# Kernel tuning notes

Hardware: AMD Instinct MI355X
Metric: run time of the kernel (lower is better)

## Reference

```python
import jax, jax.numpy as jnp
import numpy as np


def _rope_tables(T, half):
    # theta_i = 10000^(-i/half), standard RoPE frequencies for head_size=2*half
    thetas = 10000.0 ** (-jnp.arange(half, dtype=jnp.float32) / half)  # (half,)
    ang = jnp.arange(T, dtype=jnp.float32)[:, None] * thetas[None, :]  # (T, half)
    return jnp.sin(ang), jnp.cos(ang)


def _apply_rope(x, sin, cos):
    # x: (B, H, T, hs); sin/cos: (T, hs//2). Interleaved pair rotation.
    xe = x[..., 0::2]
    xo = x[..., 1::2]
    s = sin[None, None, :, :]
    c = cos[None, None, :, :]
    re = xe * c - xo * s
    ro = xe * s + xo * c
    return jnp.stack([re, ro], axis=-1).reshape(x.shape)


def setup_inputs() -> dict:
    key = jax.random.key(0)
    ks = jax.random.split(key, 5)
    B, T, C, H = 4, 2048, 1024, 16
    scale = 1.0 / np.sqrt(C)
    x = jax.random.normal(ks[0], (B, T, C), dtype=jnp.float32)
    Wqkv = jax.random.normal(ks[1], (C, 3 * C), dtype=jnp.float32) * scale
    bqkv = jax.random.normal(ks[2], (3 * C,), dtype=jnp.float32) * 0.01
    Wout = jax.random.normal(ks[3], (C, C), dtype=jnp.float32) * scale
    bout = jax.random.normal(ks[4], (C,), dtype=jnp.float32) * 0.01
    return {"x": x, "Wqkv": Wqkv, "bqkv": bqkv, "Wout": Wout, "bout": bout,
            "num_heads": H}


def reference(x, Wqkv, bqkv, Wout, bout, num_heads) -> jnp.ndarray:
    B, T, C = x.shape
    H = num_heads
    hs = C // H
    norm = 1.0 / np.sqrt(hs)

    qkv = x @ Wqkv + bqkv                       # (B, T, 3C)
    qkv = qkv.reshape(B, T, 3, H, hs)
    qkv = jnp.transpose(qkv, (0, 3, 2, 1, 4))   # (B, H, 3, T, hs) = transpose(1,3)
    q, k, v = qkv[:, :, 0], qkv[:, :, 1], qkv[:, :, 2]  # each (B, H, T, hs)

    sin, cos = _rope_tables(T, hs // 2)
    q = _apply_rope(q, sin, cos)
    k = _apply_rope(k, sin, cos)

    att = jnp.einsum('bhqd,bhkd->bhqk', q, k) * norm  # (B, H, T, T)
    causal = jnp.triu(jnp.ones((T, T), dtype=bool), k=1)
    att = jnp.where(causal[None, None], -jnp.inf, att)
    att_prob = jax.nn.softmax(att, axis=-1)

    out = jnp.einsum('bhqk,bhkd->bhqd', att_prob, v)  # (B, H, T, hs)
    out = jnp.transpose(out, (0, 2, 1, 3)).reshape(B, T, C)
    return out @ Wout + bout
```

## Files before the change

kernel.cpp:

```cpp
#include <hip/hip_runtime.h>
#include <math.h>

#define B_   4
#define T_   2048
#define C_   1024
#define H_   16
#define HS   64
#define HALF 32
#define QKV_N (3 * C_)
#define M_    (B_ * T_)

using bf16x8 = __attribute__((ext_vector_type(8))) short;
using f32x4  = __attribute__((ext_vector_type(4))) float;
using f32x16 = __attribute__((ext_vector_type(16))) float;
using u16x4  = __attribute__((ext_vector_type(4))) unsigned short;

__device__ __forceinline__ unsigned short f2bf(float f) {
    unsigned u = __builtin_bit_cast(unsigned, f);
    u = (u + 0x7FFFu + ((u >> 16) & 1u)) >> 16;
    return (unsigned short)u;
}
__device__ __forceinline__ float bf2f(unsigned short b) {
    return __builtin_bit_cast(float, (unsigned)b << 16);
}
__device__ __forceinline__ unsigned cvtpk_bf16(float lo, float hi_) {
    unsigned r;
    asm("v_cvt_pk_bf16_f32 %0, %1, %2" : "=v"(r) : "v"(lo), "v"(hi_));
    return r;
}
__device__ __forceinline__ void gload16(const void* g, void* l) {
    __builtin_amdgcn_global_load_lds(
        (const __attribute__((address_space(1))) unsigned int*)g,
        (__attribute__((address_space(3))) unsigned int*)l, 16, 0, 0);
}
#define WAIT_VMCNT_8() asm volatile("s_waitcnt vmcnt(8)" ::: "memory")
#define WAIT_VMCNT_0() asm volatile("s_waitcnt vmcnt(0)" ::: "memory")

__global__ __launch_bounds__(256) void prep_kernel(
    const float* __restrict__ in, unsigned short* __restrict__ out,
    float2* __restrict__ tab)
{
    const int bid = blockIdx.x;
    if (bid < 4096) {
        const size_t i = ((size_t)bid * 256 + threadIdx.x) * 8;
        const float4 a = *reinterpret_cast<const float4*>(&in[i]);
        const float4 b = *reinterpret_cast<const float4*>(&in[i + 4]);
        bf16x8 v;
        v[0] = f2bf(a.x); v[1] = f2bf(a.y); v[2] = f2bf(a.z); v[3] = f2bf(a.w);
        v[4] = f2bf(b.x); v[5] = f2bf(b.y); v[6] = f2bf(b.z); v[7] = f2bf(b.w);
        *reinterpret_cast<bf16x8*>(&out[i]) = v;
    } else {
        const int idx = (bid - 4096) * 256 + threadIdx.x;
        const int t = idx / HALF;
        const int i = idx % HALF;
        const float theta = powf(10000.0f, -(float)i / (float)HALF);
        const float ang = (float)t * theta;
        float sn, cs;
        sincosf(ang, &sn, &cs);
        tab[idx] = make_float2(sn, cs);
    }
}

__global__ __launch_bounds__(256) void wtrans_kernel(
    const float* __restrict__ Wqkv, const float* __restrict__ Wout,
    unsigned short* __restrict__ Wqkvt, unsigned short* __restrict__ Woutt)
{
    __shared__ float tile[32][33];
    const int bid = blockIdx.x;
    const float* W;
    unsigned short* Wt;
    int N, k0, n0;
    if (bid < 3072) {
        W = Wqkv; Wt = Wqkvt; N = QKV_N;
        n0 = (bid % 96) * 32; k0 = (bid / 96) * 32;
    } else {
        const int r2 = bid - 3072;
        W = Wout; Wt = Woutt; N = C_;
        n0 = (r2 % 32) * 32; k0 = (r2 / 32) * 32;
    }
    const int K = C_;
    const int r = threadIdx.x / 32;
    const int c = threadIdx.x % 32;
    #pragma unroll
    for (int it = 0; it < 4; ++it)
        tile[r + it * 8][c] = W[(size_t)(k0 + r + it * 8) * N + n0 + c];
    __syncthreads();
    #pragma unroll
    for (int it = 0; it < 4; ++it)
        Wt[(size_t)(n0 + r + it * 8) * K + k0 + c] = f2bf(tile[c][r + it * 8]);
}

template <int N, int K, bool BF16OUT, bool ROPE, bool VSPLIT>
__global__ __launch_bounds__(256, 4) void gemm_mfma_kernel(
    const unsigned short* __restrict__ A, const unsigned short* __restrict__ Bt,
    const float* __restrict__ bias, const float2* __restrict__ tab,
    void* __restrict__ Cout, unsigned short* __restrict__ vt, int nbx, int nby)
{
    __shared__ unsigned short As[128 * 32];
    __shared__ unsigned short Bs[128 * 32];

    const int tid  = threadIdx.x;
    const int lane = tid & 63;
    const int wave = tid >> 6;
    const int wr   = wave >> 1;
    const int wc   = wave & 1;
    const int l15  = lane & 15;
    const int l4   = lane >> 4;

    const int bid  = blockIdx.x;
    const int xcd  = bid & 7;
    const int w    = bid >> 3;
    const int cpr  = nbx >> 1;
    const int rpr  = nby >> 2;
    const int by   = ((xcd >> 1) * rpr) + (w / cpr);
    const int bx   = ((xcd & 1) * cpr) + (w % cpr);
    const int row0 = by * 128;
    const int col0 = bx * 128;

    f32x4 acc[4][4] = {};

    const int ar = tid >> 2, ac = (tid & 3) * 8;
    const unsigned short* ap = &A[(size_t)(row0 + ar) * K + ac];
    const unsigned short* bp = &Bt[(size_t)(col0 + ar) * K + ac];

    for (int it = 0; it < K / 32; ++it) {
        gload16(ap,          &As[tid * 8]);
        gload16(ap + 64 * K, &As[(tid + 256) * 8]);
        gload16(bp,          &Bs[tid * 8]);
        gload16(bp + 64 * K, &Bs[(tid + 256) * 8]);
        __syncthreads();

        bf16x8 a[4], b[4];
        #pragma unroll
        for (int mi = 0; mi < 4; ++mi)
            a[mi] = *reinterpret_cast<const bf16x8*>(
                &As[(wr * 64 + mi * 16 + l15) * 32 + l4 * 8]);
        #pragma unroll
        for (int nj = 0; nj < 4; ++nj)
            b[nj] = *reinterpret_cast<const bf16x8*>(
                &Bs[(wc * 64 + nj * 16 + l15) * 32 + l4 * 8]);
        #pragma unroll
        for (int mi = 0; mi < 4; ++mi)
            #pragma unroll
            for (int nj = 0; nj < 4; ++nj)
                acc[mi][nj] = __builtin_amdgcn_mfma_f32_16x16x32_bf16(
                    a[mi], b[nj], acc[mi][nj], 0, 0, 0);
        __syncthreads();
        ap += 32;
        bp += 32;
    }

    float bv[4];
    #pragma unroll
    for (int nj = 0; nj < 4; ++nj)
        bv[nj] = bias[col0 + wc * 64 + nj * 16 + l15];

    if (VSPLIT && col0 >= 2 * C_) {
        #pragma unroll
        for (int mi = 0; mi < 4; ++mi) {
            const int rowb = row0 + wr * 64 + mi * 16 + l4 * 4;
            const int b  = rowb >> 11;
            const int t0 = rowb & (T_ - 1);
            #pragma unroll
            for (int nj = 0; nj < 4; ++nj) {
                const int cv = col0 - 2 * C_ + wc * 64 + nj * 16 + l15;
                u16x4 pack;
                #pragma unroll
                for (int r = 0; r < 4; ++r)
                    pack[r] = f2bf(acc[mi][nj][r] + bv[nj]);
                *reinterpret_cast<u16x4*>(
                    &vt[((size_t)(b * H_ * HS + cv)) * T_ + t0]) = pack;
            }
        }
        return;
    }

    const bool doRope = ROPE && (col0 < 2 * C_);

    #pragma unroll
    for (int mi = 0; mi < 4; ++mi) {
        #pragma unroll
        for (int r = 0; r < 4; ++r) {
            const int row = row0 + wr * 64 + mi * 16 + l4 * 4 + r;
            const int t   = row & (T_ - 1);
            #pragma unroll
            for (int nj = 0; nj < 4; ++nj) {
                const int col = col0 + wc * 64 + nj * 16 + l15;
                float v = acc[mi][nj][r] + bv[nj];
                if (doRope) {
                    const float partner = __shfl_xor(v, 1);
                    const float2 sc = tab[t * HALF + ((col & 63) >> 1)];
                    v = v * sc.y + ((col & 1) ? partner : -partner) * sc.x;
                }
                if (BF16OUT)
                    ((unsigned short*)Cout)[(size_t)row * N + col] = f2bf(v);
                else
                    ((float*)Cout)[(size_t)row * N + col] = v;
            }
        }
    }
}

__global__ __launch_bounds__(256, 2) void attn_mfma4_kernel(
    const unsigned short* __restrict__ qkv,
    const unsigned short* __restrict__ vt,
    unsigned short* __restrict__ out)
{
    __shared__ unsigned short Ks[2][128 * 64];
    __shared__ unsigned short Vs[2][64 * 128];

    const int idx = blockIdx.x;
    const int bh  = idx & 63;
    const int qp  = idx >> 6;
    const int b   = bh >> 4;
    const int h   = bh & 15;
    const int qtA = qp;
    const int qtB = 15 - qp;

    const int tid  = threadIdx.x;
    const int lane = tid & 63;
    const int w    = tid >> 6;
    const int l31  = lane & 31;
    const int hi   = lane >> 5;

    const int qwA = qtA * 128 + w * 32;
    const int qgA = qwA + l31;
    const int qwB = qtB * 128 + w * 32;
    const int qgB = qwB + l31;

    bf16x8 aqA[4], aqB[4];
    {
        const unsigned short* qpA = &qkv[(size_t)(b * T_ + qgA) * QKV_N + h * HS + hi * 8];
        const unsigned short* qpB = &qkv[(size_t)(b * T_ + qgB) * QKV_N + h * HS + hi * 8];
        #pragma unroll
        for (int kc = 0; kc < 4; ++kc) {
            aqA[kc] = *reinterpret_cast<const bf16x8*>(qpA + kc * 16);
            aqB[kc] = *reinterpret_cast<const bf16x8*>(qpB + kc * 16);
        }
    }

    f32x16 accA0 = {}, accA1 = {}, accB0 = {}, accB1 = {};
    float mA = -INFINITY, lA = 0.f, mB = -INFINITY, lB = 0.f;

    const float SCALE = 0.18033688011112042f;

    auto stageKV = [&](int buf, int it) {
        #pragma unroll
        for (int n = 0; n < 4; ++n) {
            const int r  = n * 32 + (tid >> 3);
            const int sk = ((tid & 7) ^ (r & 7)) * 8;
            gload16(&qkv[(size_t)(b * T_ + it * 128 + r) * QKV_N + C_ + h * HS + sk],
                    &Ks[buf][(n * 256 + tid) * 8]);
        }
        #pragma unroll
        for (int n = 0; n < 4; ++n) {
            const int d  = n * 16 + (tid >> 4);
            const int sv = ((tid & 15) ^ (d & 7)) * 8;
            gload16(&vt[((size_t)(bh * HS + d)) * T_ + it * 128 + sv],
                    &Vs[buf][(n * 256 + tid) * 8]);
        }
    };

    auto process = [&](const unsigned short* Kb, const unsigned short* Vb,
                       const bf16x8* aq, f32x16& a0, f32x16& a1,
                       float& mval, float& lval, int qw, int qg,
                       int sub, int kbase) {
        f32x16 st0 = {}, st1 = {};
        #pragma unroll
        for (int kc = 0; kc < 4; ++kc) {
            const int bo = kc * 32 + hi * 16;
            const int r0 = sub * 64 + l31;
            const bf16x8 ak0 = *reinterpret_cast<const bf16x8*>(
                &Kb[r0 * 64 + ((bo ^ ((r0 & 7) << 4)) >> 1)]);
            st0 = __builtin_amdgcn_mfma_f32_32x32x16_bf16(ak0, aq[kc], st0, 0, 0, 0);
            const int r1 = r0 + 32;
            const bf16x8 ak1 = *reinterpret_cast<const bf16x8*>(
                &Kb[r1 * 64 + ((bo ^ ((r1 & 7) << 4)) >> 1)]);
            st1 = __builtin_amdgcn_mfma_f32_32x32x16_bf16(ak1, aq[kc], st1, 0, 0, 0);
        }

        float p[32];
        if (kbase + 63 > qw) {
            #pragma unroll
            for (int r = 0; r < 16; ++r) {
                const int j0 = kbase + (r & 3) + 8 * (r >> 2) + 4 * hi;
                p[r]      = (j0      <= qg) ? st0[r] * SCALE : -INFINITY;
                p[r + 16] = (j0 + 32 <= qg) ? st1[r] * SCALE : -INFINITY;
            }
        } else {
            #pragma unroll
            for (int r = 0; r < 16; ++r) {
                p[r]      = st0[r] * SCALE;
                p[r + 16] = st1[r] * SCALE;
            }
        }

        float tm = p[0];
        #pragma unroll
        for (int r = 1; r < 32; ++r) tm = fmaxf(tm, p[r]);
        tm = fmaxf(tm, __shfl_xor(tm, 32));

        const bool upd = (tm > mval + 8.f);
        if (__ballot(upd)) {
            const float nm = upd ? tm : mval;
            const float sf = exp2f(mval - nm);
            lval *= sf;
            #pragma unroll
            for (int r = 0; r < 16; ++r) { a0[r] *= sf; a1[r] *= sf; }
            mval = nm;
        }

        float rs = 0.f;
        #pragma unroll
        for (int r = 0; r < 32; ++r) { p[r] = exp2f(p[r] - mval); rs += p[r]; }
        rs += __shfl_xor(rs, 32);
        lval += rs;

        #pragma unroll
        for (int jt = 0; jt < 2; ++jt) {
            #pragma unroll
            for (int c = 0; c < 2; ++c) {
                const int base = jt * 16 + c * 8;
                const unsigned pa = cvtpk_bf16(p[base + 0], p[base + 1]);
                const unsigned pb = cvtpk_bf16(p[base + 2], p[base + 3]);
                const unsigned pc = cvtpk_bf16(p[base + 4], p[base + 5]);
                const unsigned pd = cvtpk_bf16(p[base + 6], p[base + 7]);
                const unsigned pas = (unsigned)__shfl_xor((int)pa, 32);
                const unsigned pbs = (unsigned)__shfl_xor((int)pb, 32);
                const unsigned pcs = (unsigned)__shfl_xor((int)pc, 32);
                const unsigned pds = (unsigned)__shfl_xor((int)pd, 32);
                int4 bw;
                bw.x = (int)(hi ? pcs : pa);
                bw.y = (int)(hi ? pds : pb);
                bw.z = (int)(hi ? pc  : pas);
                bw.w = (int)(hi ? pd  : pbs);
                const bf16x8 bfrag = __builtin_bit_cast(bf16x8, bw);

                const int lslot = sub * 8 + (jt * 2 + c) * 2 + hi;
                const int d0 = l31;
                const bf16x8 av0 = *reinterpret_cast<const bf16x8*>(
                    &Vb[d0 * 128 + (lslot ^ (d0 & 7)) * 8]);
                a0 = __builtin_amdgcn_mfma_f32_32x32x16_bf16(av0, bfrag, a0, 0, 0, 0);
                const int d1 = 32 + l31;
                const bf16x8 av1 = *reinterpret_cast<const bf16x8*>(
                    &Vb[d1 * 128 + (lslot ^ (d1 & 7)) * 8]);
                a1 = __builtin_amdgcn_mfma_f32_32x32x16_bf16(av1, bfrag, a1, 0, 0, 0);
            }
        }
    };

    const int nIter = qtB + 1;
    stageKV(0, 0);
    for (int it = 0; it < nIter; ++it) {
        const int cur = it & 1;
        __builtin_amdgcn_sched_barrier(0);
        if (it + 1 < nIter) {
            stageKV(cur ^ 1, it + 1);
            WAIT_VMCNT_8();
        } else {
            WAIT_VMCNT_0();
        }
        __builtin_amdgcn_s_barrier();
        __builtin_amdgcn_sched_barrier(0);

        const unsigned short* Kb = &Ks[cur][0];
        const unsigned short* Vb = &Vs[cur][0];
        #pragma unroll
        for (int sub = 0; sub < 2; ++sub) {
            const int kbase = it * 128 + sub * 64;
            if (kbase <= qwA + 31)
                process(Kb, Vb, aqA, accA0, accA1, mA, lA, qwA, qgA, sub, kbase);
            if (kbase <= qwB + 31)
                process(Kb, Vb, aqB, accB0, accB1, mB, lB, qwB, qgB, sub, kbase);
        }
        __builtin_amdgcn_sched_barrier(0);
        __builtin_amdgcn_s_barrier();
    }

    {
        const float inv = 1.0f / lA;
        unsigned short* orow = &out[(size_t)(b * T_ + qgA) * C_ + h * HS];
        #pragma unroll
        for (int g = 0; g < 4; ++g) {
            uint2 wv;
            wv.x = cvtpk_bf16(accA0[4 * g + 0] * inv, accA0[4 * g + 1] * inv);
            wv.y = cvtpk_bf16(accA0[4 * g + 2] * inv, accA0[4 * g + 3] * inv);
            *reinterpret_cast<uint2*>(&orow[8 * g + 4 * hi]) = wv;
            uint2 wv1;
            wv1.x = cvtpk_bf16(accA1[4 * g + 0] * inv, accA1[4 * g + 1] * inv);
            wv1.y = cvtpk_bf16(accA1[4 * g + 2] * inv, accA1[4 * g + 3] * inv);
            *reinterpret_cast<uint2*>(&orow[32 + 8 * g + 4 * hi]) = wv1;
        }
    }
    {
        const float inv = 1.0f / lB;
        unsigned short* orow = &out[(size_t)(b * T_ + qgB) * C_ + h * HS];
        #pragma unroll
        for (int g = 0; g < 4; ++g) {
            uint2 wv;
            wv.x = cvtpk_bf16(accB0[4 * g + 0] * inv, accB0[4 * g + 1] * inv);
            wv.y = cvtpk_bf16(accB0[4 * g + 2] * inv, accB0[4 * g + 3] * inv);
            *reinterpret_cast<uint2*>(&orow[8 * g + 4 * hi]) = wv;
            uint2 wv1;
            wv1.x = cvtpk_bf16(accB1[4 * g + 0] * inv, accB1[4 * g + 1] * inv);
            wv1.y = cvtpk_bf16(accB1[4 * g + 2] * inv, accB1[4 * g + 3] * inv);
            *reinterpret_cast<uint2*>(&orow[32 + 8 * g + 4 * hi]) = wv1;
        }
    }
}

extern "C" void kernel_launch(void* const* d_in, const int* in_sizes, int n_in,
                              void* d_out, int out_size, void* d_ws, size_t ws_size,
                              hipStream_t stream)
{
    const float* x    = (const float*)d_in[0];
    const float* Wqkv = (const float*)d_in[1];
    const float* bqkv = (const float*)d_in[2];
    const float* Wout = (const float*)d_in[3];
    const float* bout = (const float*)d_in[4];
    float* out = (float*)d_out;

    char* ws = (char*)d_ws;
    unsigned short* qkvb  = (unsigned short*)ws;
    unsigned short* xb    = (unsigned short*)(ws + 50331648);
    unsigned short* attnb = (unsigned short*)(ws + 67108864);
    unsigned short* vt_g  = (unsigned short*)(ws + 83886080);
    unsigned short* Wqkvt = (unsigned short*)(ws + 100663296);
    unsigned short* Woutt = (unsigned short*)(ws + 106954752);
    float2* tab           = (float2*)(ws + 109051904);

    prep_kernel<<<4352, 256, 0, stream>>>(x, xb, tab);
    wtrans_kernel<<<4096, 256, 0, stream>>>(Wqkv, Wout, Wqkvt, Woutt);

    gemm_mfma_kernel<QKV_N, C_, true, true, true>
        <<<(M_ / 128) * (QKV_N / 128), 256, 0, stream>>>(
        xb, Wqkvt, bqkv, tab, qkvb, vt_g, QKV_N / 128, M_ / 128);

    attn_mfma4_kernel<<<B_ * H_ * (T_ / 256), 256, 0, stream>>>(qkvb, vt_g, attnb);

    gemm_mfma_kernel<C_, C_, false, false, false>
        <<<(M_ / 128) * (C_ / 128), 256, 0, stream>>>(
        attnb, Woutt, bout, nullptr, out, nullptr, C_ / 128, M_ / 128);
}
```

Measured before the change: 189.6 us.

## Process full 128-key tiles per softmax step and fold Q scale into QKV GEMM

The attention inner step now computes a full 128-key score tile (four MFMA accumulators) per online-softmax update instead of two 64-key halves, halving the number of max/rescale passes. The softmax scale is folded into Q during the QKV GEMM epilogue, which removes per-element multiplies in attention. It also uses hardware exp2, max3 reductions, permlane32_swap in place of cross-half shuffles, and s_setprio around MFMA bursts. The larger score tile raises register pressure under the 2-blocks-per-CU launch bound.

```diff
diff --git a/kernel.cpp b/kernel.cpp
--- a/kernel.cpp
+++ b/kernel.cpp
@@ -14,6 +14,7 @@
 using f32x4  = __attribute__((ext_vector_type(4))) float;
 using f32x16 = __attribute__((ext_vector_type(16))) float;
 using u16x4  = __attribute__((ext_vector_type(4))) unsigned short;
+using u32x2  = __attribute__((ext_vector_type(2))) unsigned int;
 
 __device__ __forceinline__ unsigned short f2bf(float f) {
     unsigned u = __builtin_bit_cast(unsigned, f);
@@ -35,6 +36,15 @@
 }
 #define WAIT_VMCNT_8() asm volatile("s_waitcnt vmcnt(8)" ::: "memory")
 #define WAIT_VMCNT_0() asm volatile("s_waitcnt vmcnt(0)" ::: "memory")
+
+#if __has_builtin(__builtin_amdgcn_exp2f)
+#define EXP2(x) __builtin_amdgcn_exp2f(x)
+#else
+#define EXP2(x) exp2f(x)
+#endif
+#define FMAX3(a, b, c) fmaxf(fmaxf((a), (b)), (c))
+
+#define QSCALE 0.18033688011112042f
 
 __global__ __launch_bounds__(256) void prep_kernel(
     const float* __restrict__ in, unsigned short* __restrict__ out,
@@ -176,6 +186,7 @@
     }
 
     const bool doRope = ROPE && (col0 < 2 * C_);
+    const bool doScaleQ = ROPE && (col0 < C_);
 
     #pragma unroll
     for (int mi = 0; mi < 4; ++mi) {
@@ -192,6 +203,7 @@
                     const float2 sc = tab[t * HALF + ((col & 63) >> 1)];
                     v = v * sc.y + ((col & 1) ? partner : -partner) * sc.x;
                 }
+                if (doScaleQ) v *= QSCALE;
                 if (BF16OUT)
                     ((unsigned short*)Cout)[(size_t)row * N + col] = f2bf(v);
                 else
@@ -201,7 +213,7 @@
     }
 }
 
-__global__ __launch_bounds__(256, 2) void attn_mfma4_kernel(
+__global__ __launch_bounds__(256, 2) void attn_mfma5_kernel(
     const unsigned short* __restrict__ qkv,
     const unsigned short* __restrict__ vt,
     unsigned short* __restrict__ out)
@@ -242,8 +254,6 @@
     f32x16 accA0 = {}, accA1 = {}, accB0 = {}, accB1 = {};
     float mA = -INFINITY, lA = 0.f, mB = -INFINITY, lB = 0.f;
 
-    const float SCALE = 0.18033688011112042f;
-
     auto stageKV = [&](int buf, int it) {
         #pragma unroll
         for (int n = 0; n < 4; ++n) {
@@ -263,88 +273,110 @@
 
     auto process = [&](const unsigned short* Kb, const unsigned short* Vb,
                        const bf16x8* aq, f32x16& a0, f32x16& a1,
-                       float& mval, float& lval, int qw, int qg,
-                       int sub, int kbase) {
-        f32x16 st0 = {}, st1 = {};
+                       float& mval, float& lval, int qw, int qg, int kbase) {
+        f32x16 s[4] = {};
+        __builtin_amdgcn_s_setprio(1);
         #pragma unroll
         for (int kc = 0; kc < 4; ++kc) {
             const int bo = kc * 32 + hi * 16;
-            const int r0 = sub * 64 + l31;
-            const bf16x8 ak0 = *reinterpret_cast<const bf16x8*>(
-                &Kb[r0 * 64 + ((bo ^ ((r0 & 7) << 4)) >> 1)]);
-            st0 = __builtin_amdgcn_mfma_f32_32x32x16_bf16(ak0, aq[kc], st0, 0, 0, 0);
-            const int r1 = r0 + 32;
-            const bf16x8 ak1 = *reinterpret_cast<const bf16x8*>(
-                &Kb[r1 * 64 + ((bo ^ ((r1 & 7) << 4)) >> 1)]);
-            st1 = __builtin_amdgcn_mfma_f32_32x32x16_bf16(ak1, aq[kc], st1, 0, 0, 0);
-        }
-
-        float p[32];
-        if (kbase + 63 > qw) {
-            #pragma unroll
-            for (int r = 0; r < 16; ++r) {
-                const int j0 = kbase + (r & 3) + 8 * (r >> 2) + 4 * hi;
-                p[r]      = (j0      <= qg) ? st0[r] * SCALE : -INFINITY;
-                p[r + 16] = (j0 + 32 <= qg) ? st1[r] * SCALE : -INFINITY;
+            #pragma unroll
+            for (int g = 0; g < 4; ++g) {
+                const int rj = g * 32 + l31;
+                const bf16x8 ak = *reinterpret_cast<const bf16x8*>(
+                    &Kb[rj * 64 + ((bo ^ ((rj & 7) << 4)) >> 1)]);
+                s[g] = __builtin_amdgcn_mfma_f32_32x32x16_bf16(ak, aq[kc], s[g], 0, 0, 0);
             }
-        } else {
-            #pragma unroll
-            for (int r = 0; r < 16; ++r) {
-                p[r]      = st0[r] * SCALE;
-                p[r + 16] = st1[r] * SCALE;
+        }
+        __builtin_amdgcn_s_setprio(0);
+
+        if (kbase + 127 > qw) {
+            #pragma unroll
+            for (int g = 0; g < 4; ++g) {
+                #pragma unroll
+                for (int r = 0; r < 16; ++r) {
+                    const int j0 = kbase + g * 32 + (r & 3) + 8 * (r >> 2) + 4 * hi;
+                    if (j0 > qg) s[g][r] = -INFINITY;
+                }
             }
         }
 
-        float tm = p[0];
-        #pragma unroll
-        for (int r = 1; r < 32; ++r) tm = fmaxf(tm, p[r]);
+        float tg[4];
+        #pragma unroll
+        for (int g = 0; g < 4; ++g) {
+            const float v0 = FMAX3(s[g][0],  s[g][1],  s[g][2]);
+            const float v1 = FMAX3(s[g][3],  s[g][4],  s[g][5]);
+            const float v2 = FMAX3(s[g][6],  s[g][7],  s[g][8]);
+            const float v3 = FMAX3(s[g][9],  s[g][10], s[g][11]);
+            const float v4 = FMAX3(s[g][12], s[g][13], s[g][14]);
+            tg[g] = fmaxf(FMAX3(v0, v1, v2), FMAX3(v3, v4, s[g][15]));
+        }
+        float tm = fmaxf(fmaxf(tg[0], tg[1]), fmaxf(tg[2], tg[3]));
         tm = fmaxf(tm, __shfl_xor(tm, 32));
 
         const bool upd = (tm > mval + 8.f);
         if (__ballot(upd)) {
             const float nm = upd ? tm : mval;
-            const float sf = exp2f(mval - nm);
+            const float sf = EXP2(mval - nm);
             lval *= sf;
             #pragma unroll
             for (int r = 0; r < 16; ++r) { a0[r] *= sf; a1[r] *= sf; }
             mval = nm;
         }
 
-        float rs = 0.f;
-        #pragma unroll
-        for (int r = 0; r < 32; ++r) { p[r] = exp2f(p[r] - mval); rs += p[r]; }
+        float rs0 = 0.f, rs1 = 0.f, rs2 = 0.f, rs3 = 0.f;
+        #pragma unroll
+        for (int r = 0; r < 16; ++r) {
+            s[0][r] = EXP2(s[0][r] - mval); rs0 += s[0][r];
+            s[1][r] = EXP2(s[1][r] - mval); rs1 += s[1][r];
+            s[2][r] = EXP2(s[2][r] - mval); rs2 += s[2][r];
+            s[3][r] = EXP2(s[3][r] - mval); rs3 += s[3][r];
+        }
+        float rs = (rs0 + rs1) + (rs2 + rs3);
         rs += __shfl_xor(rs, 32);
         lval += rs;
 
         #pragma unroll
-        for (int jt = 0; jt < 2; ++jt) {
-            #pragma unroll
-            for (int c = 0; c < 2; ++c) {
-                const int base = jt * 16 + c * 8;
-                const unsigned pa = cvtpk_bf16(p[base + 0], p[base + 1]);
-                const unsigned pb = cvtpk_bf16(p[base + 2], p[base + 3]);
-                const unsigned pc = cvtpk_bf16(p[base + 4], p[base + 5]);
-                const unsigned pd = cvtpk_bf16(p[base + 6], p[base + 7]);
-                const unsigned pas = (unsigned)__shfl_xor((int)pa, 32);
-                const unsigned pbs = (unsigned)__shfl_xor((int)pb, 32);
-                const unsigned pcs = (unsigned)__shfl_xor((int)pc, 32);
-                const unsigned pds = (unsigned)__shfl_xor((int)pd, 32);
-                int4 bw;
-                bw.x = (int)(hi ? pcs : pa);
-                bw.y = (int)(hi ? pds : pb);
-                bw.z = (int)(hi ? pc  : pas);
-                bw.w = (int)(hi ? pd  : pbs);
-                const bf16x8 bfrag = __builtin_bit_cast(bf16x8, bw);
-
-                const int lslot = sub * 8 + (jt * 2 + c) * 2 + hi;
-                const int d0 = l31;
-                const bf16x8 av0 = *reinterpret_cast<const bf16x8*>(
-                    &Vb[d0 * 128 + (lslot ^ (d0 & 7)) * 8]);
-                a0 = __builtin_amdgcn_mfma_f32_32x32x16_bf16(av0, bfrag, a0, 0, 0, 0);
-                const int d1 = 32 + l31;
-                const bf16x8 av1 = *reinterpret_cast<const bf16x8*>(
-                    &Vb[d1 * 128 + (lslot ^ (d1 & 7)) * 8]);
-                a1 = __builtin_amdgcn_mfma_f32_32x32x16_bf16(av1, bfrag, a1, 0, 0, 0);
+        for (int g2 = 0; g2 < 2; ++g2) {
+            #pragma unroll
+            for (int jt = 0; jt < 2; ++jt) {
+                const int g = g2 * 2 + jt;
+                #pragma unroll
+                for (int c = 0; c < 2; ++c) {
+                    const int e = c * 8;
+                    const unsigned pa = cvtpk_bf16(s[g][e + 0], s[g][e + 1]);
+                    const unsigned pb = cvtpk_bf16(s[g][e + 2], s[g][e + 3]);
+                    const unsigned pc = cvtpk_bf16(s[g][e + 4], s[g][e + 5]);
+                    const unsigned pd = cvtpk_bf16(s[g][e + 6], s[g][e + 7]);
+                    int4 bw;
+#if __has_builtin(__builtin_amdgcn_permlane32_swap)
+                    const u32x2 rx = __builtin_amdgcn_permlane32_swap(pa, pc, false, false);
+                    const u32x2 ry = __builtin_amdgcn_permlane32_swap(pb, pd, false, false);
+                    bw.x = (int)rx[0]; bw.y = (int)ry[0];
+                    bw.z = (int)rx[1]; bw.w = (int)ry[1];
+#else
+                    const unsigned pas = (unsigned)__shfl_xor((int)pa, 32);
+                    const unsigned pbs = (unsigned)__shfl_xor((int)pb, 32);
+                    const unsigned pcs = (unsigned)__shfl_xor((int)pc, 32);
+                    const unsigned pds = (unsigned)__shfl_xor((int)pd, 32);
+                    bw.x = (int)(hi ? pcs : pa);
+                    bw.y = (int)(hi ? pds : pb);
+                    bw.z = (int)(hi ? pc  : pas);
+                    bw.w = (int)(hi ? pd  : pbs);
+#endif
+                    const bf16x8 bfrag = __builtin_bit_cast(bf16x8, bw);
+
+                    const int lslot = g2 * 8 + (jt * 2 + c) * 2 + hi;
+                    const int d0 = l31;
+                    const bf16x8 av0 = *reinterpret_cast<const bf16x8*>(
+                        &Vb[d0 * 128 + (lslot ^ (d0 & 7)) * 8]);
+                    const int d1 = 32 + l31;
+                    const bf16x8 av1 = *reinterpret_cast<const bf16x8*>(
+                        &Vb[d1 * 128 + (lslot ^ (d1 & 7)) * 8]);
+                    __builtin_amdgcn_s_setprio(1);
+                    a0 = __builtin_amdgcn_mfma_f32_32x32x16_bf16(av0, bfrag, a0, 0, 0, 0);
+                    a1 = __builtin_amdgcn_mfma_f32_32x32x16_bf16(av1, bfrag, a1, 0, 0, 0);
+                    __builtin_amdgcn_s_setprio(0);
+                }
             }
         }
     };
@@ -365,14 +397,11 @@
 
         const unsigned short* Kb = &Ks[cur][0];
         const unsigned short* Vb = &Vs[cur][0];
-        #pragma unroll
-        for (int sub = 0; sub < 2; ++sub) {
-            const int kbase = it * 128 + sub * 64;
-            if (kbase <= qwA + 31)
-                process(Kb, Vb, aqA, accA0, accA1, mA, lA, qwA, qgA, sub, kbase);
-            if (kbase <= qwB + 31)
-                process(Kb, Vb, aqB, accB0, accB1, mB, lB, qwB, qgB, sub, kbase);
-        }
+        const int kbase = it * 128;
+        if (kbase <= qwA + 31)
+            process(Kb, Vb, aqA, accA0, accA1, mA, lA, qwA, qgA, kbase);
+        if (kbase <= qwB + 31)
+            process(Kb, Vb, aqB, accB0, accB1, mB, lB, qwB, qgB, kbase);
         __builtin_amdgcn_sched_barrier(0);
         __builtin_amdgcn_s_barrier();
     }
@@ -436,7 +465,7 @@
         <<<(M_ / 128) * (QKV_N / 128), 256, 0, stream>>>(
         xb, Wqkvt, bqkv, tab, qkvb, vt_g, QKV_N / 128, M_ / 128);
 
-    attn_mfma4_kernel<<<B_ * H_ * (T_ / 256), 256, 0, stream>>>(qkvb, vt_g, attnb);
+    attn_mfma5_kernel<<<B_ * H_ * (T_ / 256), 256, 0, stream>>>(qkvb, vt_g, attnb);
 
     gemm_mfma_kernel<C_, C_, false, false, false>
         <<<(M_ / 128) * (C_ / 128), 256, 0, stream>>>(
```

Measured after the change: 169.8 us. -10.5%, faster.
